# Kernel tuning notes

Hardware: AMD Instinct MI355X
Metric: run time of the kernel (lower is better)

Reference implementation:

```python
import jax, jax.numpy as jnp
import numpy as np

B, S, D, H = 1, 4096, 512, 8
HD = D // H  # head_dims = 64


def setup_inputs() -> dict:
    key = jax.random.key(0)
    ks = jax.random.split(key, 12)
    scale = 0.02
    query = jax.random.normal(ks[0], (B, S, D), dtype=jnp.float32)
    key_t = jax.random.normal(ks[1], (B, S, D), dtype=jnp.float32)
    value = jax.random.normal(ks[2], (B, S, D), dtype=jnp.float32)
    mask = jax.random.randint(ks[3], (B, 1, S, S), 0, 2, dtype=jnp.int32)
    # per-head projection params (torch Linear: y = x @ W.T + b)
    Wq = jax.random.normal(ks[4], (HD, HD), dtype=jnp.float32) * scale
    bq = jax.random.normal(ks[5], (HD,), dtype=jnp.float32) * scale
    Wk = jax.random.normal(ks[6], (HD, HD), dtype=jnp.float32) * scale
    bk = jax.random.normal(ks[7], (HD,), dtype=jnp.float32) * scale
    Wv = jax.random.normal(ks[8], (HD, HD), dtype=jnp.float32) * scale
    bv = jax.random.normal(ks[9], (HD,), dtype=jnp.float32) * scale
    Wfc = jax.random.normal(ks[10], (D, D), dtype=jnp.float32) * scale
    bfc = jax.random.normal(ks[11], (D,), dtype=jnp.float32) * scale
    return {"query": query, "key": key_t, "value": value, "mask": mask,
            "Wq": Wq, "bq": bq, "Wk": Wk, "bk": bk, "Wv": Wv, "bv": bv,
            "Wfc": Wfc, "bfc": bfc}


def reference(query, key, value, mask, Wq, bq, Wk, bk, Wv, bv, Wfc, bfc):
    Batch, q_len, _ = query.shape
    k_len = key.shape[1]
    # reshape to [b, s, h, d] then apply per-head linear projections
    q = query.reshape(Batch, q_len, H, HD) @ Wq.T + bq
    k = key.reshape(Batch, k_len, H, HD) @ Wk.T + bk
    v = value.reshape(Batch, k_len, H, HD) @ Wv.T + bv
    # raw scores [b, h, q, k]; mask applied BEFORE scaling (as in original)
    score = jnp.einsum('bqhd,bkhd->bhqk', q, k)
    score = jnp.where(mask == 0, jnp.float32(-1e20), score)
    attn = jax.nn.softmax(score / jnp.sqrt(jnp.float32(HD)), axis=-1)
    out = jnp.einsum('bhqv,bvhd->bqhd', attn, v).reshape(Batch, q_len, D)
    return out @ Wfc.T + bfc
```

## Files before the change

kernel.cpp:

```cpp
#include <hip/hip_runtime.h>
#include <hip/hip_bf16.h>

#define S_LEN 4096
#define DMODEL 512
#define NHEAD 8
#define HDIM 64

typedef __bf16 bf16x8 __attribute__((ext_vector_type(8)));
typedef __bf16 bf16x4 __attribute__((ext_vector_type(4)));
typedef float f32x4 __attribute__((ext_vector_type(4)));

#define S2EXP 0.18033688011112042f

__device__ __forceinline__ void gload_lds16(const void* g, void* l) {
    __builtin_amdgcn_global_load_lds((const __attribute__((address_space(1))) void*)g,
                                     (__attribute__((address_space(3))) void*)l, 16, 0, 0);
}
__device__ __forceinline__ void gload_lds4(const void* g, void* l) {
    __builtin_amdgcn_global_load_lds((const __attribute__((address_space(1))) void*)g,
                                     (__attribute__((address_space(3))) void*)l, 4, 0, 0);
}

__global__ __launch_bounds__(256) void proj_all_kernel(const float* __restrict__ xq,
                                                       const float* __restrict__ xk,
                                                       const float* __restrict__ xv,
                                                       const float* __restrict__ Wq,
                                                       const float* __restrict__ bq,
                                                       const float* __restrict__ Wk,
                                                       const float* __restrict__ bk,
                                                       const float* __restrict__ Wv,
                                                       const float* __restrict__ bv,
                                                       __bf16* __restrict__ yq,
                                                       __bf16* __restrict__ yk,
                                                       __bf16* __restrict__ vt) {
    __shared__ float T[64][65];
    int bid = blockIdx.x;
    int t = threadIdx.x, wave = t >> 6, lane = t & 63, lg = lane >> 4, lc = lane & 15;
    if (bid < 512) {
        int r0 = bid * 64 + wave * 16;
        const float* xrq = xq + (size_t)(r0 + lc) * 64 + lg * 8;
        const float* xrk = xk + (size_t)(r0 + lc) * 64 + lg * 8;
        bf16x8 aq[2], ak[2];
#pragma unroll
        for (int c = 0; c < 2; ++c) {
            f32x4 u0 = *(const f32x4*)(xrq + c * 32);
            f32x4 u1 = *(const f32x4*)(xrq + c * 32 + 4);
            f32x4 v0 = *(const f32x4*)(xrk + c * 32);
            f32x4 v1 = *(const f32x4*)(xrk + c * 32 + 4);
            bf16x8 a, b;
#pragma unroll
            for (int j = 0; j < 4; ++j) {
                a[j] = (__bf16)u0[j]; a[4 + j] = (__bf16)u1[j];
                b[j] = (__bf16)v0[j]; b[4 + j] = (__bf16)v1[j];
            }
            aq[c] = a; ak[c] = b;
        }
#pragma unroll
        for (int nt = 0; nt < 4; ++nt) {
            const float* wq = Wq + (size_t)(nt * 16 + lc) * 64 + lg * 8;
            const float* wk = Wk + (size_t)(nt * 16 + lc) * 64 + lg * 8;
            f32x4 cq = {0, 0, 0, 0}, ck = {0, 0, 0, 0};
#pragma unroll
            for (int c = 0; c < 2; ++c) {
                f32x4 u0 = *(const f32x4*)(wq + c * 32);
                f32x4 u1 = *(const f32x4*)(wq + c * 32 + 4);
                f32x4 v0 = *(const f32x4*)(wk + c * 32);
                f32x4 v1 = *(const f32x4*)(wk + c * 32 + 4);
                bf16x8 bw, bw2;
#pragma unroll
                for (int j = 0; j < 4; ++j) {
                    bw[j] = (__bf16)u0[j]; bw[4 + j] = (__bf16)u1[j];
                    bw2[j] = (__bf16)v0[j]; bw2[4 + j] = (__bf16)v1[j];
                }
                cq = __builtin_amdgcn_mfma_f32_16x16x32_bf16(aq[c], bw, cq, 0, 0, 0);
                ck = __builtin_amdgcn_mfma_f32_16x16x32_bf16(ak[c], bw2, ck, 0, 0, 0);
            }
            float bqv = bq[nt * 16 + lc], bkv = bk[nt * 16 + lc];
#pragma unroll
            for (int r = 0; r < 4; ++r) {
                yq[(size_t)(r0 + lg * 4 + r) * 64 + nt * 16 + lc] = (__bf16)((cq[r] + bqv) * S2EXP);
                yk[(size_t)(r0 + lg * 4 + r) * 64 + nt * 16 + lc] = (__bf16)(ck[r] + bkv);
            }
        }
    } else {
        int vb = bid - 512;
        int h = vb & 7, s0 = (vb >> 3) * 64;
        const float* xr = xv + ((size_t)(s0 + wave * 16 + lc) * 8 + h) * 64 + lg * 8;
        bf16x8 av[2];
#pragma unroll
        for (int c = 0; c < 2; ++c) {
            f32x4 u0 = *(const f32x4*)(xr + c * 32);
            f32x4 u1 = *(const f32x4*)(xr + c * 32 + 4);
            bf16x8 a;
#pragma unroll
            for (int j = 0; j < 4; ++j) { a[j] = (__bf16)u0[j]; a[4 + j] = (__bf16)u1[j]; }
            av[c] = a;
        }
#pragma unroll
        for (int nt = 0; nt < 4; ++nt) {
            const float* wv = Wv + (size_t)(nt * 16 + lc) * 64 + lg * 8;
            f32x4 cv = {0, 0, 0, 0};
#pragma unroll
            for (int c = 0; c < 2; ++c) {
                f32x4 u0 = *(const f32x4*)(wv + c * 32);
                f32x4 u1 = *(const f32x4*)(wv + c * 32 + 4);
                bf16x8 bw;
#pragma unroll
                for (int j = 0; j < 4; ++j) { bw[j] = (__bf16)u0[j]; bw[4 + j] = (__bf16)u1[j]; }
                cv = __builtin_amdgcn_mfma_f32_16x16x32_bf16(av[c], bw, cv, 0, 0, 0);
            }
            float bvv = bv[nt * 16 + lc];
#pragma unroll
            for (int r = 0; r < 4; ++r) T[wave * 16 + lg * 4 + r][nt * 16 + lc] = cv[r] + bvv;
        }
        __syncthreads();
        int d = t >> 2, qr = t & 3;
        bf16x8 w0, w1;
#pragma unroll
        for (int i = 0; i < 8; ++i) {
            w0[i] = (__bf16)T[qr * 16 + i][d];
            w1[i] = (__bf16)T[qr * 16 + 8 + i][d];
        }
        __bf16* dst = vt + ((size_t)h * 64 + d) * 4096 + s0 + qr * 16;
        *(bf16x8*)(dst) = w0;
        *(bf16x8*)(dst + 8) = w1;
    }
}

__global__ __launch_bounds__(256) void prep_kernel(const int* __restrict__ mask,
                                                   unsigned int* __restrict__ pack,
                                                   const float* __restrict__ Wfc,
                                                   __bf16* __restrict__ wfc_bf) {
    int bid = blockIdx.x;
    int t = threadIdx.x;
    if (bid < 2048) {
        int lane = t & 63;
        int wid = bid * 4 + (t >> 6);
#pragma unroll 4
        for (int it = 0; it < 32; ++it) {
            int gw = wid * 32 + it;
            int qi = gw >> 6, seg = gw & 63;
            unsigned long long bits = __ballot(mask[(size_t)qi * 4096 + seg * 64 + lane] != 0);
            if (lane == 0)
                *(unsigned long long*)(&pack[(size_t)qi * 128 + seg * 2]) = bits;
        }
    } else {
        int b = bid - 2048;
        const f32x4* s4 = (const f32x4*)Wfc;
#pragma unroll
        for (int i = 0; i < 8; ++i) {
            int idx = (b * 8 + i) * 256 + t;
            f32x4 v = s4[idx];
            bf16x4 o;
#pragma unroll
            for (int j = 0; j < 4; ++j) o[j] = (__bf16)v[j];
            *(bf16x4*)(wfc_bf + (size_t)idx * 4) = o;
        }
    }
}

__global__ __launch_bounds__(256, 4) void attn_kernel(const __bf16* __restrict__ qb,
                                                      const __bf16* __restrict__ kb,
                                                      const __bf16* __restrict__ vt,
                                                      const unsigned int* __restrict__ mp,
                                                      int split_steps,
                                                      float* __restrict__ opart,
                                                      float* __restrict__ stats,
                                                      __bf16* __restrict__ ao) {
    int bid = blockIdx.x;
    int h = bid & 7, qt = (bid >> 3) & 63, sp = bid >> 9;
    int kv0 = sp * split_steps * 32;
    int nsteps = split_steps;
    int t = threadIdx.x, wave = t >> 6, lane = t & 63, lg = lane >> 4, lc = lane & 15;
    int q0 = qt * 64 + wave * 16;

    __shared__ __bf16 Kt[4][32 * 64];
    __shared__ __bf16 Vt[4][64 * 32];
    __shared__ __bf16 P[4][16 * 32];
    __shared__ unsigned int Mld[4][64];

    int srK = lane >> 3;
    int cgK = (lane & 7) ^ srK;
    int srV = lane >> 2;
    int cgV = ((lane & 3) - ((lane >> 3) & 3)) & 3;

    const __bf16* qrow = qb + ((size_t)(q0 + lc) * 8 + h) * 64 + lg * 8;
    bf16x8 qf0 = *(const bf16x8*)(qrow);
    bf16x8 qf1 = *(const bf16x8*)(qrow + 32);

    bf16x8 onesf;
#pragma unroll
    for (int j = 0; j < 8; ++j) onesf[j] = (__bf16)1.0f;

    f32x4 o0 = {0,0,0,0}, o1 = {0,0,0,0}, o2 = {0,0,0,0}, o3 = {0,0,0,0};
    f32x4 l_acc = {0,0,0,0};

    const __bf16* vbase = vt + (size_t)h * 64 * 4096;
    const unsigned int* mbase = mp + (size_t)(qt * 64 + lane) * 128 + (kv0 >> 5);

    int rotP = (lc >> 1) & 3;
    int lg4 = lg * 4;

#define STAGE(tt, B)                                                                       \
    {                                                                                      \
        if (wave == 0) gload_lds4(mbase + (tt), &Mld[B][0]);                               \
        gload_lds16(kb + (size_t)(kv0 + (tt) * 32 + wave * 8 + srK) * 512 + h * 64 + cgK * 8, \
                    &Kt[B][wave * 512]);                                                   \
        gload_lds16(vbase + (size_t)(wave * 16 + srV) * 4096 + kv0 + (tt) * 32 + cgV * 8,  \
                    &Vt[B][wave * 512]);                                                   \
    }

    STAGE(0, 0)
    STAGE(1, 1)
    asm volatile("s_waitcnt vmcnt(0)" ::: "memory");
    __builtin_amdgcn_s_barrier();

#define ATTN_STEP(s, C, G)                                                                 \
    {                                                                                      \
        if ((s) + 2 < nsteps) STAGE((s) + 2, G)                                            \
        asm volatile("s_waitcnt vmcnt(4)" ::: "memory");                                   \
        __builtin_amdgcn_s_barrier();                                                      \
        unsigned int mws = Mld[C][wave * 16 + lc] >> lg4;                                  \
        const char* Kb = (const char*)&Kt[C][0];                                           \
        f32x4 sc0 = {0,0,0,0}, sc1 = {0,0,0,0};                                            \
        {                                                                                  \
            int row = lc, sw = (row & 7) << 4;                                             \
            bf16x8 kf0 = *(const bf16x8*)(Kb + ((row * 128 + lg * 16) ^ sw));              \
            bf16x8 kf1 = *(const bf16x8*)(Kb + ((row * 128 + 64 + lg * 16) ^ sw));         \
            sc0 = __builtin_amdgcn_mfma_f32_16x16x32_bf16(kf0, qf0, sc0, 0, 0, 0);         \
            sc0 = __builtin_amdgcn_mfma_f32_16x16x32_bf16(kf1, qf1, sc0, 0, 0, 0);         \
        }                                                                                  \
        {                                                                                  \
            int row = 16 + lc, sw = (row & 7) << 4;                                        \
            bf16x8 kf0 = *(const bf16x8*)(Kb + ((row * 128 + lg * 16) ^ sw));              \
            bf16x8 kf1 = *(const bf16x8*)(Kb + ((row * 128 + 64 + lg * 16) ^ sw));         \
            sc1 = __builtin_amdgcn_mfma_f32_16x16x32_bf16(kf0, qf0, sc1, 0, 0, 0);         \
            sc1 = __builtin_amdgcn_mfma_f32_16x16x32_bf16(kf1, qf1, sc1, 0, 0, 0);         \
        }                                                                                  \
        char* pbase = (char*)&P[wave][0];                                                  \
        {                                                                                  \
            bf16x4 pk0, pk1;                                                               \
            _Pragma("unroll")                                                              \
            for (int r = 0; r < 4; ++r) {                                                  \
                float pa = __builtin_amdgcn_exp2f(sc0[r]);                                 \
                int sa = __builtin_amdgcn_sbfe((int)mws, r, 1);                            \
                pk0[r] = (__bf16)__int_as_float(__float_as_int(pa) & sa);                  \
                float pb = __builtin_amdgcn_exp2f(sc1[r]);                                 \
                int sb = __builtin_amdgcn_sbfe((int)mws, 16 + r, 1);                       \
                pk1[r] = (__bf16)__int_as_float(__float_as_int(pb) & sb);                  \
            }                                                                              \
            int ph0 = (((lg >> 1)) + rotP) & 3;                                            \
            int ph1 = ((2 + (lg >> 1)) + rotP) & 3;                                        \
            *(bf16x4*)(pbase + lc * 64 + ph0 * 16 + (lg & 1) * 8) = pk0;                   \
            *(bf16x4*)(pbase + lc * 64 + ph1 * 16 + (lg & 1) * 8) = pk1;                   \
        }                                                                                  \
        const char* Vb = (const char*)&Vt[C][0];                                           \
        bf16x8 pf = *(const bf16x8*)(pbase + (lc * 64 + (((lg + rotP) & 3) * 16)));        \
        l_acc = __builtin_amdgcn_mfma_f32_16x16x32_bf16(pf, onesf, l_acc, 0, 0, 0);        \
        _Pragma("unroll")                                                                  \
        for (int dt = 0; dt < 4; ++dt) {                                                   \
            int row = dt * 16 + lc;                                                        \
            bf16x8 vf = *(const bf16x8*)(Vb + (row * 64 + (((lg + rotP) & 3) * 16)));      \
            if (dt == 0) o0 = __builtin_amdgcn_mfma_f32_16x16x32_bf16(pf, vf, o0, 0, 0, 0);\
            if (dt == 1) o1 = __builtin_amdgcn_mfma_f32_16x16x32_bf16(pf, vf, o1, 0, 0, 0);\
            if (dt == 2) o2 = __builtin_amdgcn_mfma_f32_16x16x32_bf16(pf, vf, o2, 0, 0, 0);\
            if (dt == 3) o3 = __builtin_amdgcn_mfma_f32_16x16x32_bf16(pf, vf, o3, 0, 0, 0);\
        }                                                                                  \
    }

    for (int s = 0; s < nsteps; s += 4) {
        ATTN_STEP(s + 0, 0, 2)
        ATTN_STEP(s + 1, 1, 3)
        ATTN_STEP(s + 2, 2, 0)
        ATTN_STEP(s + 3, 3, 1)
    }
#undef ATTN_STEP
#undef STAGE

    if (opart) {
        if (lc == 0) {
#pragma unroll
            for (int r = 0; r < 4; ++r)
                stats[(size_t)sp * 32768 + (size_t)(q0 + lg * 4 + r) * 8 + h] = l_acc[r];
        }
#pragma unroll
        for (int r = 0; r < 4; ++r) {
            size_t rh = (size_t)sp * 32768 + (size_t)(q0 + lg * 4 + r) * 8 + h;
            float* dst = opart + rh * 64;
            dst[0 * 16 + lc] = o0[r];
            dst[1 * 16 + lc] = o1[r];
            dst[2 * 16 + lc] = o2[r];
            dst[3 * 16 + lc] = o3[r];
        }
    } else {
#pragma unroll
        for (int r = 0; r < 4; ++r) {
            float inv = 1.0f / l_acc[r];
            int row = q0 + lg * 4 + r;
            __bf16* dst = ao + (size_t)row * 512 + h * 64;
            dst[0 * 16 + lc] = (__bf16)(o0[r] * inv);
            dst[1 * 16 + lc] = (__bf16)(o1[r] * inv);
            dst[2 * 16 + lc] = (__bf16)(o2[r] * inv);
            dst[3 * 16 + lc] = (__bf16)(o3[r] * inv);
        }
    }
}

__global__ __launch_bounds__(256) void combine_kernel(const float* __restrict__ opart,
                                                      const float* __restrict__ stats,
                                                      __bf16* __restrict__ ao, int nsplit) {
    int t = threadIdx.x, lane = t & 63, w = t >> 6;
    int rh = blockIdx.x * 4 + w;
    float L = 0.f, acc = 0.f;
#pragma unroll 2
    for (int sp = 0; sp < nsplit; ++sp) {
        L += stats[(size_t)sp * 32768 + rh];
        acc += opart[((size_t)sp * 32768 + rh) * 64 + lane];
    }
    int row = rh >> 3, h = rh & 7;
    ao[(size_t)row * 512 + h * 64 + lane] = (__bf16)(acc / L);
}

__global__ __launch_bounds__(256) void fc_kernel(const __bf16* __restrict__ ao,
                                                 const __bf16* __restrict__ Wb,
                                                 const float* __restrict__ bfc,
                                                 float* __restrict__ out) {
    int bid = blockIdx.x;
    int stile = bid >> 3, nt = bid & 7;
    int t = threadIdx.x, wave = t >> 6, lane = t & 63, lg = lane >> 4, lc = lane & 15;
    int s0 = stile * 64 + wave * 16;
    int n0 = nt * 64;
    f32x4 c0 = {0,0,0,0}, c1 = {0,0,0,0}, c2 = {0,0,0,0}, c3 = {0,0,0,0};
    for (int k0 = 0; k0 < 512; k0 += 32) {
        bf16x8 af = *(const bf16x8*)(ao + (size_t)(s0 + lc) * 512 + k0 + lg * 8);
        const __bf16* wb = Wb + k0 + lg * 8;
        c0 = __builtin_amdgcn_mfma_f32_16x16x32_bf16(af, *(const bf16x8*)(wb + (size_t)(n0 + 0 * 16 + lc) * 512), c0, 0, 0, 0);
        c1 = __builtin_amdgcn_mfma_f32_16x16x32_bf16(af, *(const bf16x8*)(wb + (size_t)(n0 + 1 * 16 + lc) * 512), c1, 0, 0, 0);
        c2 = __builtin_amdgcn_mfma_f32_16x16x32_bf16(af, *(const bf16x8*)(wb + (size_t)(n0 + 2 * 16 + lc) * 512), c2, 0, 0, 0);
        c3 = __builtin_amdgcn_mfma_f32_16x16x32_bf16(af, *(const bf16x8*)(wb + (size_t)(n0 + 3 * 16 + lc) * 512), c3, 0, 0, 0);
    }
#pragma unroll
    for (int r = 0; r < 4; ++r) {
        int row = s0 + lg * 4 + r;
        float* dst = out + (size_t)row * 512 + n0;
        dst[0 * 16 + lc] = c0[r] + bfc[n0 + 0 * 16 + lc];
        dst[1 * 16 + lc] = c1[r] + bfc[n0 + 1 * 16 + lc];
        dst[2 * 16 + lc] = c2[r] + bfc[n0 + 2 * 16 + lc];
        dst[3 * 16 + lc] = c3[r] + bfc[n0 + 3 * 16 + lc];
    }
}

extern "C" void kernel_launch(void* const* d_in, const int* in_sizes, int n_in,
                              void* d_out, int out_size, void* d_ws, size_t ws_size,
                              hipStream_t stream) {
    const float* query = (const float*)d_in[0];
    const float* key   = (const float*)d_in[1];
    const float* value = (const float*)d_in[2];
    const int*   mask  = (const int*)d_in[3];
    const float* Wq  = (const float*)d_in[4];
    const float* bq  = (const float*)d_in[5];
    const float* Wk  = (const float*)d_in[6];
    const float* bk  = (const float*)d_in[7];
    const float* Wv  = (const float*)d_in[8];
    const float* bv  = (const float*)d_in[9];
    const float* Wfc = (const float*)d_in[10];
    const float* bfc = (const float*)d_in[11];

    char* ws = (char*)d_ws;
    const size_t MB = 1024 * 1024;
    __bf16* q_bf   = (__bf16*)(ws + 0 * MB);
    __bf16* k_bf   = (__bf16*)(ws + 4 * MB);
    __bf16* vt     = (__bf16*)(ws + 8 * MB);
    __bf16* ao     = (__bf16*)(ws + 12 * MB);
    __bf16* wfc_bf = (__bf16*)(ws + 16 * MB);
    unsigned int* mpack = (unsigned int*)(ws + 17 * MB);
    const size_t base = 19 * MB;
    int nsplit = (ws_size >= base + 2 * (8 * MB) + 2 * 131072) ? 2 : 1;
    float* opart = (float*)(ws + base);
    float* stats = (float*)(ws + base + (size_t)nsplit * 8 * MB);

    proj_all_kernel<<<1024, 256, 0, stream>>>(query, key, value, Wq, bq, Wk, bk, Wv, bv,
                                              q_bf, k_bf, vt);
    prep_kernel<<<2080, 256, 0, stream>>>(mask, mpack, Wfc, wfc_bf);
    if (nsplit > 1) {
        attn_kernel<<<512 * nsplit, 256, 0, stream>>>(q_bf, k_bf, vt, mpack,
                                                      S_LEN / nsplit / 32, opart, stats, ao);
        combine_kernel<<<8192, 256, 0, stream>>>(opart, stats, ao, nsplit);
    } else {
        attn_kernel<<<512, 256, 0, stream>>>(q_bf, k_bf, vt, mpack,
                                             128, nullptr, nullptr, ao);
    }
    fc_kernel<<<512, 256, 0, stream>>>(ao, wfc_bf, bfc, (float*)d_out);
}
```

Before: 123.6 us.

## Process two query tiles per wave and split KV three ways in attention

```diff
diff --git a/kernel.cpp b/kernel.cpp
--- a/kernel.cpp
+++ b/kernel.cpp
@@ -159,7 +159,7 @@
     }
 }
 
-__global__ __launch_bounds__(256, 4) void attn_kernel(const __bf16* __restrict__ qb,
+__global__ __launch_bounds__(256, 3) void attn_kernel(const __bf16* __restrict__ qb,
                                                       const __bf16* __restrict__ kb,
                                                       const __bf16* __restrict__ vt,
                                                       const unsigned int* __restrict__ mp,
@@ -168,46 +168,50 @@
                                                       float* __restrict__ stats,
                                                       __bf16* __restrict__ ao) {
     int bid = blockIdx.x;
-    int h = bid & 7, qt = (bid >> 3) & 63, sp = bid >> 9;
+    int h = bid & 7, qtb = (bid >> 3) & 31, sp = bid >> 8;
     int kv0 = sp * split_steps * 32;
-    int nsteps = split_steps;
+    int nsteps = min(split_steps, 128 - sp * split_steps);
     int t = threadIdx.x, wave = t >> 6, lane = t & 63, lg = lane >> 4, lc = lane & 15;
-    int q0 = qt * 64 + wave * 16;
+    int q0 = qtb * 128 + wave * 32;
 
     __shared__ __bf16 Kt[4][32 * 64];
     __shared__ __bf16 Vt[4][64 * 32];
-    __shared__ __bf16 P[4][16 * 32];
-    __shared__ unsigned int Mld[4][64];
+    __shared__ __bf16 P[4][32 * 32];
+    __shared__ unsigned int Mld[4][128];
 
     int srK = lane >> 3;
     int cgK = (lane & 7) ^ srK;
     int srV = lane >> 2;
     int cgV = ((lane & 3) - ((lane >> 3) & 3)) & 3;
 
-    const __bf16* qrow = qb + ((size_t)(q0 + lc) * 8 + h) * 64 + lg * 8;
-    bf16x8 qf0 = *(const bf16x8*)(qrow);
-    bf16x8 qf1 = *(const bf16x8*)(qrow + 32);
+    const __bf16* qr0 = qb + ((size_t)(q0 + lc) * 8 + h) * 64 + lg * 8;
+    const __bf16* qr1 = qb + ((size_t)(q0 + 16 + lc) * 8 + h) * 64 + lg * 8;
+    bf16x8 qf00 = *(const bf16x8*)(qr0);
+    bf16x8 qf01 = *(const bf16x8*)(qr0 + 32);
+    bf16x8 qf10 = *(const bf16x8*)(qr1);
+    bf16x8 qf11 = *(const bf16x8*)(qr1 + 32);
 
     bf16x8 onesf;
 #pragma unroll
     for (int j = 0; j < 8; ++j) onesf[j] = (__bf16)1.0f;
 
-    f32x4 o0 = {0,0,0,0}, o1 = {0,0,0,0}, o2 = {0,0,0,0}, o3 = {0,0,0,0};
-    f32x4 l_acc = {0,0,0,0};
+    f32x4 o00 = {0,0,0,0}, o01 = {0,0,0,0}, o02 = {0,0,0,0}, o03 = {0,0,0,0};
+    f32x4 o10 = {0,0,0,0}, o11 = {0,0,0,0}, o12 = {0,0,0,0}, o13 = {0,0,0,0};
+    f32x4 lac0 = {0,0,0,0}, lac1 = {0,0,0,0};
 
     const __bf16* vbase = vt + (size_t)h * 64 * 4096;
-    const unsigned int* mbase = mp + (size_t)(qt * 64 + lane) * 128 + (kv0 >> 5);
+    const unsigned int* mbase = mp + (size_t)(qtb * 128 + wave * 64 + lane) * 128 + (kv0 >> 5);
 
     int rotP = (lc >> 1) & 3;
     int lg4 = lg * 4;
 
-#define STAGE(tt, B)                                                                       \
-    {                                                                                      \
-        if (wave == 0) gload_lds4(mbase + (tt), &Mld[B][0]);                               \
+#define STAGE(tt, B)                                                                          \
+    {                                                                                         \
+        if (wave < 2) gload_lds4(mbase + (tt), &Mld[B][wave * 64]);                           \
         gload_lds16(kb + (size_t)(kv0 + (tt) * 32 + wave * 8 + srK) * 512 + h * 64 + cgK * 8, \
-                    &Kt[B][wave * 512]);                                                   \
-        gload_lds16(vbase + (size_t)(wave * 16 + srV) * 4096 + kv0 + (tt) * 32 + cgV * 8,  \
-                    &Vt[B][wave * 512]);                                                   \
+                    &Kt[B][wave * 512]);                                                      \
+        gload_lds16(vbase + (size_t)(wave * 16 + srV) * 4096 + kv0 + (tt) * 32 + cgV * 8,     \
+                    &Vt[B][wave * 512]);                                                      \
     }
 
     STAGE(0, 0)
@@ -215,93 +219,130 @@
     asm volatile("s_waitcnt vmcnt(0)" ::: "memory");
     __builtin_amdgcn_s_barrier();
 
-#define ATTN_STEP(s, C, G)                                                                 \
-    {                                                                                      \
-        if ((s) + 2 < nsteps) STAGE((s) + 2, G)                                            \
-        asm volatile("s_waitcnt vmcnt(4)" ::: "memory");                                   \
-        __builtin_amdgcn_s_barrier();                                                      \
-        unsigned int mws = Mld[C][wave * 16 + lc] >> lg4;                                  \
-        const char* Kb = (const char*)&Kt[C][0];                                           \
-        f32x4 sc0 = {0,0,0,0}, sc1 = {0,0,0,0};                                            \
-        {                                                                                  \
-            int row = lc, sw = (row & 7) << 4;                                             \
-            bf16x8 kf0 = *(const bf16x8*)(Kb + ((row * 128 + lg * 16) ^ sw));              \
-            bf16x8 kf1 = *(const bf16x8*)(Kb + ((row * 128 + 64 + lg * 16) ^ sw));         \
-            sc0 = __builtin_amdgcn_mfma_f32_16x16x32_bf16(kf0, qf0, sc0, 0, 0, 0);         \
-            sc0 = __builtin_amdgcn_mfma_f32_16x16x32_bf16(kf1, qf1, sc0, 0, 0, 0);         \
-        }                                                                                  \
-        {                                                                                  \
-            int row = 16 + lc, sw = (row & 7) << 4;                                        \
-            bf16x8 kf0 = *(const bf16x8*)(Kb + ((row * 128 + lg * 16) ^ sw));              \
-            bf16x8 kf1 = *(const bf16x8*)(Kb + ((row * 128 + 64 + lg * 16) ^ sw));         \
-            sc1 = __builtin_amdgcn_mfma_f32_16x16x32_bf16(kf0, qf0, sc1, 0, 0, 0);         \
-            sc1 = __builtin_amdgcn_mfma_f32_16x16x32_bf16(kf1, qf1, sc1, 0, 0, 0);         \
-        }                                                                                  \
-        char* pbase = (char*)&P[wave][0];                                                  \
-        {                                                                                  \
-            bf16x4 pk0, pk1;                                                               \
-            _Pragma("unroll")                                                              \
-            for (int r = 0; r < 4; ++r) {                                                  \
-                float pa = __builtin_amdgcn_exp2f(sc0[r]);                                 \
-                int sa = __builtin_amdgcn_sbfe((int)mws, r, 1);                            \
-                pk0[r] = (__bf16)__int_as_float(__float_as_int(pa) & sa);                  \
-                float pb = __builtin_amdgcn_exp2f(sc1[r]);                                 \
-                int sb = __builtin_amdgcn_sbfe((int)mws, 16 + r, 1);                       \
-                pk1[r] = (__bf16)__int_as_float(__float_as_int(pb) & sb);                  \
-            }                                                                              \
-            int ph0 = (((lg >> 1)) + rotP) & 3;                                            \
-            int ph1 = ((2 + (lg >> 1)) + rotP) & 3;                                        \
-            *(bf16x4*)(pbase + lc * 64 + ph0 * 16 + (lg & 1) * 8) = pk0;                   \
-            *(bf16x4*)(pbase + lc * 64 + ph1 * 16 + (lg & 1) * 8) = pk1;                   \
-        }                                                                                  \
-        const char* Vb = (const char*)&Vt[C][0];                                           \
-        bf16x8 pf = *(const bf16x8*)(pbase + (lc * 64 + (((lg + rotP) & 3) * 16)));        \
-        l_acc = __builtin_amdgcn_mfma_f32_16x16x32_bf16(pf, onesf, l_acc, 0, 0, 0);        \
-        _Pragma("unroll")                                                                  \
-        for (int dt = 0; dt < 4; ++dt) {                                                   \
-            int row = dt * 16 + lc;                                                        \
-            bf16x8 vf = *(const bf16x8*)(Vb + (row * 64 + (((lg + rotP) & 3) * 16)));      \
-            if (dt == 0) o0 = __builtin_amdgcn_mfma_f32_16x16x32_bf16(pf, vf, o0, 0, 0, 0);\
-            if (dt == 1) o1 = __builtin_amdgcn_mfma_f32_16x16x32_bf16(pf, vf, o1, 0, 0, 0);\
-            if (dt == 2) o2 = __builtin_amdgcn_mfma_f32_16x16x32_bf16(pf, vf, o2, 0, 0, 0);\
-            if (dt == 3) o3 = __builtin_amdgcn_mfma_f32_16x16x32_bf16(pf, vf, o3, 0, 0, 0);\
-        }                                                                                  \
-    }
-
-    for (int s = 0; s < nsteps; s += 4) {
+#define ATTN_STEP(s, C, G)                                                                    \
+    {                                                                                         \
+        STAGE(min((s) + 2, nsteps - 1), G)                                                    \
+        asm volatile("s_waitcnt vmcnt(4)" ::: "memory");                                      \
+        __builtin_amdgcn_s_barrier();                                                         \
+        unsigned int mw0 = Mld[C][wave * 32 + lc] >> lg4;                                     \
+        unsigned int mw1 = Mld[C][wave * 32 + 16 + lc] >> lg4;                                \
+        const char* Kb = (const char*)&Kt[C][0];                                              \
+        f32x4 s00 = {0,0,0,0}, s01 = {0,0,0,0}, s10 = {0,0,0,0}, s11 = {0,0,0,0};             \
+        {                                                                                     \
+            int row = lc, sw = (row & 7) << 4;                                                \
+            bf16x8 ka = *(const bf16x8*)(Kb + ((row * 128 + lg * 16) ^ sw));                  \
+            bf16x8 kc_ = *(const bf16x8*)(Kb + ((row * 128 + 64 + lg * 16) ^ sw));            \
+            s00 = __builtin_amdgcn_mfma_f32_16x16x32_bf16(ka, qf00, s00, 0, 0, 0);            \
+            s00 = __builtin_amdgcn_mfma_f32_16x16x32_bf16(kc_, qf01, s00, 0, 0, 0);           \
+            s01 = __builtin_amdgcn_mfma_f32_16x16x32_bf16(ka, qf10, s01, 0, 0, 0);            \
+            s01 = __builtin_amdgcn_mfma_f32_16x16x32_bf16(kc_, qf11, s01, 0, 0, 0);           \
+        }                                                                                     \
+        {                                                                                     \
+            int row = 16 + lc, sw = (row & 7) << 4;                                           \
+            bf16x8 ka = *(const bf16x8*)(Kb + ((row * 128 + lg * 16) ^ sw));                  \
+            bf16x8 kc_ = *(const bf16x8*)(Kb + ((row * 128 + 64 + lg * 16) ^ sw));            \
+            s10 = __builtin_amdgcn_mfma_f32_16x16x32_bf16(ka, qf00, s10, 0, 0, 0);            \
+            s10 = __builtin_amdgcn_mfma_f32_16x16x32_bf16(kc_, qf01, s10, 0, 0, 0);           \
+            s11 = __builtin_amdgcn_mfma_f32_16x16x32_bf16(ka, qf10, s11, 0, 0, 0);            \
+            s11 = __builtin_amdgcn_mfma_f32_16x16x32_bf16(kc_, qf11, s11, 0, 0, 0);           \
+        }                                                                                     \
+        char* pb = (char*)&P[wave][0];                                                        \
+        {                                                                                     \
+            bf16x4 k0q0, k1q0, k0q1, k1q1;                                                    \
+            _Pragma("unroll")                                                                 \
+            for (int r = 0; r < 4; ++r) {                                                     \
+                float pa = __builtin_amdgcn_exp2f(s00[r]);                                    \
+                k0q0[r] = (__bf16)__int_as_float(__float_as_int(pa) &                         \
+                                                 __builtin_amdgcn_sbfe((int)mw0, r, 1));      \
+                float pc = __builtin_amdgcn_exp2f(s10[r]);                                    \
+                k1q0[r] = (__bf16)__int_as_float(__float_as_int(pc) &                         \
+                                                 __builtin_amdgcn_sbfe((int)mw0, 16 + r, 1)); \
+                float pd = __builtin_amdgcn_exp2f(s01[r]);                                    \
+                k0q1[r] = (__bf16)__int_as_float(__float_as_int(pd) &                         \
+                                                 __builtin_amdgcn_sbfe((int)mw1, r, 1));      \
+                float pe = __builtin_amdgcn_exp2f(s11[r]);                                    \
+                k1q1[r] = (__bf16)__int_as_float(__float_as_int(pe) &                         \
+                                                 __builtin_amdgcn_sbfe((int)mw1, 16 + r, 1)); \
+            }                                                                                 \
+            int ph0 = ((lg >> 1) + rotP) & 3;                                                 \
+            int ph1 = (2 + (lg >> 1) + rotP) & 3;                                             \
+            int ib = (lg & 1) * 8;                                                            \
+            *(bf16x4*)(pb + lc * 64 + ph0 * 16 + ib) = k0q0;                                  \
+            *(bf16x4*)(pb + lc * 64 + ph1 * 16 + ib) = k1q0;                                  \
+            *(bf16x4*)(pb + 1024 + lc * 64 + ph0 * 16 + ib) = k0q1;                           \
+            *(bf16x4*)(pb + 1024 + lc * 64 + ph1 * 16 + ib) = k1q1;                           \
+        }                                                                                     \
+        int prd = lc * 64 + (((lg + rotP) & 3) * 16);                                         \
+        bf16x8 pf0 = *(const bf16x8*)(pb + prd);                                              \
+        bf16x8 pf1 = *(const bf16x8*)(pb + 1024 + prd);                                       \
+        lac0 = __builtin_amdgcn_mfma_f32_16x16x32_bf16(pf0, onesf, lac0, 0, 0, 0);            \
+        lac1 = __builtin_amdgcn_mfma_f32_16x16x32_bf16(pf1, onesf, lac1, 0, 0, 0);            \
+        const char* Vb = (const char*)&Vt[C][0];                                              \
+        {                                                                                     \
+            bf16x8 vf = *(const bf16x8*)(Vb + ((0 * 16 + lc) * 64 + (((lg + rotP) & 3) * 16)));\
+            o00 = __builtin_amdgcn_mfma_f32_16x16x32_bf16(pf0, vf, o00, 0, 0, 0);             \
+            o10 = __builtin_amdgcn_mfma_f32_16x16x32_bf16(pf1, vf, o10, 0, 0, 0);             \
+        }                                                                                     \
+        {                                                                                     \
+            bf16x8 vf = *(const bf16x8*)(Vb + ((1 * 16 + lc) * 64 + (((lg + rotP) & 3) * 16)));\
+            o01 = __builtin_amdgcn_mfma_f32_16x16x32_bf16(pf0, vf, o01, 0, 0, 0);             \
+            o11 = __builtin_amdgcn_mfma_f32_16x16x32_bf16(pf1, vf, o11, 0, 0, 0);             \
+        }                                                                                     \
+        {                                                                                     \
+            bf16x8 vf = *(const bf16x8*)(Vb + ((2 * 16 + lc) * 64 + (((lg + rotP) & 3) * 16)));\
+            o02 = __builtin_amdgcn_mfma_f32_16x16x32_bf16(pf0, vf, o02, 0, 0, 0);             \
+            o12 = __builtin_amdgcn_mfma_f32_16x16x32_bf16(pf1, vf, o12, 0, 0, 0);             \
+        }                                                                                     \
+        {                                                                                     \
+            bf16x8 vf = *(const bf16x8*)(Vb + ((3 * 16 + lc) * 64 + (((lg + rotP) & 3) * 16)));\
+            o03 = __builtin_amdgcn_mfma_f32_16x16x32_bf16(pf0, vf, o03, 0, 0, 0);             \
+            o13 = __builtin_amdgcn_mfma_f32_16x16x32_bf16(pf1, vf, o13, 0, 0, 0);             \
+        }                                                                                     \
+    }
+
+    int s = 0;
+    for (; s + 4 <= nsteps; s += 4) {
         ATTN_STEP(s + 0, 0, 2)
         ATTN_STEP(s + 1, 1, 3)
         ATTN_STEP(s + 2, 2, 0)
         ATTN_STEP(s + 3, 3, 1)
     }
+    if (s < nsteps) { ATTN_STEP(s, 0, 2) s++; }
+    if (s < nsteps) { ATTN_STEP(s, 1, 3) s++; }
+    if (s < nsteps) { ATTN_STEP(s, 2, 0) s++; }
 #undef ATTN_STEP
 #undef STAGE
 
     if (opart) {
         if (lc == 0) {
 #pragma unroll
-            for (int r = 0; r < 4; ++r)
-                stats[(size_t)sp * 32768 + (size_t)(q0 + lg * 4 + r) * 8 + h] = l_acc[r];
+            for (int r = 0; r < 4; ++r) {
+                stats[(size_t)sp * 32768 + (size_t)(q0 + lg * 4 + r) * 8 + h]      = lac0[r];
+                stats[(size_t)sp * 32768 + (size_t)(q0 + 16 + lg * 4 + r) * 8 + h] = lac1[r];
+            }
         }
 #pragma unroll
         for (int r = 0; r < 4; ++r) {
-            size_t rh = (size_t)sp * 32768 + (size_t)(q0 + lg * 4 + r) * 8 + h;
-            float* dst = opart + rh * 64;
-            dst[0 * 16 + lc] = o0[r];
-            dst[1 * 16 + lc] = o1[r];
-            dst[2 * 16 + lc] = o2[r];
-            dst[3 * 16 + lc] = o3[r];
+            size_t rh0 = (size_t)sp * 32768 + (size_t)(q0 + lg * 4 + r) * 8 + h;
+            float* d0 = opart + rh0 * 64;
+            d0[0 * 16 + lc] = o00[r]; d0[1 * 16 + lc] = o01[r];
+            d0[2 * 16 + lc] = o02[r]; d0[3 * 16 + lc] = o03[r];
+            size_t rh1 = (size_t)sp * 32768 + (size_t)(q0 + 16 + lg * 4 + r) * 8 + h;
+            float* d1 = opart + rh1 * 64;
+            d1[0 * 16 + lc] = o10[r]; d1[1 * 16 + lc] = o11[r];
+            d1[2 * 16 + lc] = o12[r]; d1[3 * 16 + lc] = o13[r];
         }
     } else {
 #pragma unroll
         for (int r = 0; r < 4; ++r) {
-            float inv = 1.0f / l_acc[r];
-            int row = q0 + lg * 4 + r;
-            __bf16* dst = ao + (size_t)row * 512 + h * 64;
-            dst[0 * 16 + lc] = (__bf16)(o0[r] * inv);
-            dst[1 * 16 + lc] = (__bf16)(o1[r] * inv);
-            dst[2 * 16 + lc] = (__bf16)(o2[r] * inv);
-            dst[3 * 16 + lc] = (__bf16)(o3[r] * inv);
+            float inv0 = 1.0f / lac0[r];
+            __bf16* d0 = ao + (size_t)(q0 + lg * 4 + r) * 512 + h * 64;
+            d0[0 * 16 + lc] = (__bf16)(o00[r] * inv0); d0[1 * 16 + lc] = (__bf16)(o01[r] * inv0);
+            d0[2 * 16 + lc] = (__bf16)(o02[r] * inv0); d0[3 * 16 + lc] = (__bf16)(o03[r] * inv0);
+            float inv1 = 1.0f / lac1[r];
+            __bf16* d1 = ao + (size_t)(q0 + 16 + lg * 4 + r) * 512 + h * 64;
+            d1[0 * 16 + lc] = (__bf16)(o10[r] * inv1); d1[1 * 16 + lc] = (__bf16)(o11[r] * inv1);
+            d1[2 * 16 + lc] = (__bf16)(o12[r] * inv1); d1[3 * 16 + lc] = (__bf16)(o13[r] * inv1);
         }
     }
 }
@@ -312,7 +353,7 @@
     int t = threadIdx.x, lane = t & 63, w = t >> 6;
     int rh = blockIdx.x * 4 + w;
     float L = 0.f, acc = 0.f;
-#pragma unroll 2
+#pragma unroll 3
     for (int sp = 0; sp < nsplit; ++sp) {
         L += stats[(size_t)sp * 32768 + rh];
         acc += opart[((size_t)sp * 32768 + rh) * 64 + lane];
@@ -375,7 +416,7 @@
     __bf16* wfc_bf = (__bf16*)(ws + 16 * MB);
     unsigned int* mpack = (unsigned int*)(ws + 17 * MB);
     const size_t base = 19 * MB;
-    int nsplit = (ws_size >= base + 2 * (8 * MB) + 2 * 131072) ? 2 : 1;
+    int nsplit = (ws_size >= base + 3 * (8 * MB) + 3 * 131072) ? 3 : 1;
     float* opart = (float*)(ws + base);
     float* stats = (float*)(ws + base + (size_t)nsplit * 8 * MB);
 
@@ -383,11 +424,11 @@
                                               q_bf, k_bf, vt);
     prep_kernel<<<2080, 256, 0, stream>>>(mask, mpack, Wfc, wfc_bf);
     if (nsplit > 1) {
-        attn_kernel<<<512 * nsplit, 256, 0, stream>>>(q_bf, k_bf, vt, mpack,
-                                                      S_LEN / nsplit / 32, opart, stats, ao);
+        attn_kernel<<<256 * nsplit, 256, 0, stream>>>(q_bf, k_bf, vt, mpack,
+                                                      43, opart, stats, ao);
         combine_kernel<<<8192, 256, 0, stream>>>(opart, stats, ao, nsplit);
     } else {
-        attn_kernel<<<512, 256, 0, stream>>>(q_bf, k_bf, vt, mpack,
+        attn_kernel<<<256, 256, 0, stream>>>(q_bf, k_bf, vt, mpack,
                                              128, nullptr, nullptr, ao);
     }
     fc_kernel<<<512, 256, 0, stream>>>(ao, wfc_bf, bfc, (float*)d_out);
```

After: 119.6 us. 1.03x faster.
